# Optimization experiments

Measured on AMD Instinct MI355X. Metric: run time of the kernel, lower is better.

Reference implementation:

```python
import jax, jax.numpy as jnp
import numpy as np

B, D_IN, D_HID, D_OUT = 32768, 512, 4096, 512
EPS = 1e-12  # F.normalize eps


def setup_inputs() -> dict:
    key = jax.random.key(0)
    ks = jax.random.split(key, 9)
    # Weights scaled up from the original 0.001 init so the norm_max clamp
    # branch is actually exercised (norms vary around the threshold).
    return {
        "x": jax.random.normal(ks[0], (B, D_IN), jnp.float32),
        "in_mean": jax.random.normal(ks[1], (D_IN,), jnp.float32) * 0.1,
        "in_std": jax.random.uniform(ks[2], (D_IN,), jnp.float32, 0.5, 1.5),
        "out_mean": jax.random.normal(ks[3], (D_OUT,), jnp.float32) * 0.1,
        "out_std": jax.random.uniform(ks[4], (D_OUT,), jnp.float32, 0.5, 1.5),
        "W1": jax.random.normal(ks[5], (D_HID, D_IN), jnp.float32) * 0.02,
        "b1": jax.random.normal(ks[6], (D_HID,), jnp.float32) * 0.001,
        "W2": jax.random.normal(ks[7], (D_OUT, D_HID), jnp.float32) * 0.02,
        "b2": jax.random.normal(ks[8], (D_OUT,), jnp.float32) * 0.001,
        "norm_max": 1,
    }


def reference(x, in_mean, in_std, out_mean, out_std, W1, b1, W2, b2, norm_max):
    norm_max = jnp.float32(norm_max)
    x_copy = x[..., :512]
    # input normalization
    xn = (x - in_mean) / in_std
    # 2-layer MLP: Linear -> ReLU -> Linear
    h = jax.nn.relu(jnp.einsum("bi,hi->bh", xn, W1) + b1)
    res = jnp.einsum("bh,oh->bo", h, W2) + b2
    # vectorized per-row norm clamp (torch loop: rescale rows with norm > norm_max)
    norms = jnp.linalg.norm(res, axis=-1, keepdims=True)  # [B,1]
    scale = norm_max / jax.lax.stop_gradient(norms)
    res = jnp.where(norms > norm_max, res * scale, res)
    # output de-normalization (torch subtracts norm_input[0] here)
    res = res * out_std + out_mean - in_mean
    # residual + L2 normalize
    mapped = res + x_copy
    mnorm = jnp.linalg.norm(mapped, axis=-1, keepdims=True)
    return mapped / jnp.maximum(mnorm, EPS)
```

## Files before the change

### kernel.cpp

```cpp
#include <hip/hip_runtime.h>
#include <hip/hip_bf16.h>

#define NB 32768
#define DIN 512
#define DHID 4096
#define DOUT 512

typedef __attribute__((ext_vector_type(8))) __bf16 bf16x8;
typedef __attribute__((ext_vector_type(4))) float f32x4;

__device__ __forceinline__ unsigned short f2bf(float f) {
  unsigned u = __builtin_bit_cast(unsigned, f);
  u += 0x7FFFu + ((u >> 16) & 1u);
  return (unsigned short)(u >> 16);
}

__device__ __forceinline__ void gload16(void* lds, const void* g) {
  __builtin_amdgcn_global_load_lds(
      (const __attribute__((address_space(1))) void*)g,
      (__attribute__((address_space(3))) void*)lds, 16, 0, 0);
}

__global__ __launch_bounds__(256) void k_prep_x(
    const float4* __restrict__ x, const float* __restrict__ mean,
    const float* __restrict__ stdv, ushort4* __restrict__ xn) {
  const int i = blockIdx.x * 256 + threadIdx.x;
  const int col = (i << 2) & (DIN - 1);
  const float4 v = x[i];
  const float4 m = *(const float4*)(mean + col);
  const float4 s = *(const float4*)(stdv + col);
  ushort4 o;
  o.x = f2bf((v.x - m.x) / s.x);
  o.y = f2bf((v.y - m.y) / s.y);
  o.z = f2bf((v.z - m.z) / s.z);
  o.w = f2bf((v.w - m.w) / s.w);
  xn[i] = o;
}

__global__ __launch_bounds__(256) void k_cvt(
    const float4* __restrict__ in, ushort4* __restrict__ out) {
  const int i = blockIdx.x * 256 + threadIdx.x;
  const float4 v = in[i];
  ushort4 o;
  o.x = f2bf(v.x); o.y = f2bf(v.y); o.z = f2bf(v.z); o.w = f2bf(v.w);
  out[i] = o;
}

template <int EPI>
__global__ __launch_bounds__(512, 2) void k_gemm(
    const unsigned short* __restrict__ A, const unsigned short* __restrict__ W,
    const float* __restrict__ bias, void* __restrict__ outp,
    const int N, const int K, const int nbn) {
  __shared__ __align__(16) char lds[3 * 49152];
  const int tid = threadIdx.x;
  const int wave = tid >> 6, lane = tid & 63;
  const int wm = wave >> 1, wn = wave & 1;
  const int lidlo = lane & 15, lidhi = lane >> 4;

  const int nwg = (int)gridDim.x;
  const int wg = (int)blockIdx.x;
  const int q = nwg >> 3, r = nwg & 7;
  const int xcd = wg & 7, loc = wg >> 3;
  const int swz = (xcd < r ? xcd * (q + 1) : r * (q + 1) + (xcd - r) * q) + loc;
  const int bm = swz / nbn, bn = swz % nbn;
  const int R0 = bm * 256, C0 = bn * 128;

  const int NT = K >> 6;
  const int dbase0 = wave * 1024;

  auto STAGE = [&](int t, int s) {
    char* as = lds + s * 49152;
    char* bs = as + 32768;
    const int k0 = t << 6;
#pragma unroll
    for (int i = 0; i < 4; ++i) {
      const int db = i * 8192 + dbase0;
      const int d = db + lane * 16;
      const int row = d >> 7;
      const int colb = (d & 127) ^ ((row & 7) << 4);
      gload16(as + db,
              (const char*)A + ((size_t)(R0 + row) * K + k0) * 2 + colb);
    }
#pragma unroll
    for (int i = 0; i < 2; ++i) {
      const int db = i * 8192 + dbase0;
      const int d = db + lane * 16;
      const int row = d >> 7;
      const int colb = (d & 127) ^ ((row & 7) << 4);
      gload16(bs + db,
              (const char*)W + ((size_t)(C0 + row) * K + k0) * 2 + colb);
    }
  };

  f32x4 acc[4][4] = {};

  STAGE(0, 0);
  STAGE(1, 1);
  asm volatile("s_waitcnt vmcnt(6)" ::: "memory");
  __builtin_amdgcn_s_barrier();

  int slot = 0;
  for (int t = 0; t < NT; ++t) {
    const int nslot = (slot == 2) ? 0 : slot + 1;
    const int sslot = (nslot == 2) ? 0 : nslot + 1;
    if (t + 2 < NT) STAGE(t + 2, sslot);

    const char* as = lds + slot * 49152;
    const char* bs = as + 32768;
    bf16x8 af[2][4], bw[2][4];
#pragma unroll
    for (int kk = 0; kk < 2; ++kk) {
#pragma unroll
      for (int i = 0; i < 4; ++i) {
        const int ra = wm * 64 + i * 16 + lidlo;
        af[kk][i] = *(const bf16x8*)(
            as + ra * 128 + ((kk * 64 + lidhi * 16) ^ ((ra & 7) << 4)));
        const int rb = wn * 64 + i * 16 + lidlo;
        bw[kk][i] = *(const bf16x8*)(
            bs + rb * 128 + ((kk * 64 + lidhi * 16) ^ ((rb & 7) << 4)));
      }
    }
    __builtin_amdgcn_s_setprio(1);
#pragma unroll
    for (int kk = 0; kk < 2; ++kk)
#pragma unroll
      for (int i = 0; i < 4; ++i)
#pragma unroll
        for (int j = 0; j < 4; ++j)
          acc[i][j] = __builtin_amdgcn_mfma_f32_16x16x32_bf16(
              af[kk][i], bw[kk][j], acc[i][j], 0, 0, 0);
    __builtin_amdgcn_s_setprio(0);

    if (t + 2 < NT) {
      asm volatile("s_waitcnt vmcnt(6)" ::: "memory");
    } else {
      asm volatile("s_waitcnt vmcnt(0)" ::: "memory");
    }
    __builtin_amdgcn_s_barrier();
    slot = nslot;
  }

  const int m0 = R0 + wm * 64 + (lidhi << 2);
  const int n0 = C0 + wn * 64 + lidlo;
#pragma unroll
  for (int j = 0; j < 4; ++j) {
    const int n = n0 + j * 16;
    const float bv = bias[n];
#pragma unroll
    for (int i = 0; i < 4; ++i) {
#pragma unroll
      for (int rr = 0; rr < 4; ++rr) {
        const int m = m0 + i * 16 + rr;
        float v = acc[i][j][rr] + bv;
        if (EPI == 0) {
          v = fmaxf(v, 0.0f);
          ((unsigned short*)outp)[(size_t)m * N + n] = f2bf(v);
        } else {
          ((float*)outp)[(size_t)m * N + n] = v;
        }
      }
    }
  }
}

__global__ __launch_bounds__(256) void k_finalize(
    float* __restrict__ res, const float* __restrict__ x,
    const float* __restrict__ out_mean, const float* __restrict__ out_std,
    const float* __restrict__ in_mean, const int* __restrict__ nmp) {
  const int wave = threadIdx.x >> 6, lane = threadIdx.x & 63;
  const size_t row = (size_t)blockIdx.x * 4 + wave;
  const float nm = (float)(*nmp);
  const size_t base = row * DOUT + (size_t)lane * 8;
  const int c = lane * 8;
  const float4 r0 = *(const float4*)(res + base);
  const float4 r1 = *(const float4*)(res + base + 4);
  float ss = r0.x * r0.x + r0.y * r0.y + r0.z * r0.z + r0.w * r0.w +
             r1.x * r1.x + r1.y * r1.y + r1.z * r1.z + r1.w * r1.w;
#pragma unroll
  for (int o = 32; o > 0; o >>= 1) ss += __shfl_xor(ss, o);
  const float rn = sqrtf(ss);
  const float sc = (rn > nm) ? (nm / rn) : 1.0f;
  const float4 os0 = *(const float4*)(out_std + c);
  const float4 os1 = *(const float4*)(out_std + c + 4);
  const float4 om0 = *(const float4*)(out_mean + c);
  const float4 om1 = *(const float4*)(out_mean + c + 4);
  const float4 im0 = *(const float4*)(in_mean + c);
  const float4 im1 = *(const float4*)(in_mean + c + 4);
  const float4 x0 = *(const float4*)(x + base);
  const float4 x1 = *(const float4*)(x + base + 4);
  float4 m0, m1;
  m0.x = r0.x * sc * os0.x + om0.x - im0.x + x0.x;
  m0.y = r0.y * sc * os0.y + om0.y - im0.y + x0.y;
  m0.z = r0.z * sc * os0.z + om0.z - im0.z + x0.z;
  m0.w = r0.w * sc * os0.w + om0.w - im0.w + x0.w;
  m1.x = r1.x * sc * os1.x + om1.x - im1.x + x1.x;
  m1.y = r1.y * sc * os1.y + om1.y - im1.y + x1.y;
  m1.z = r1.z * sc * os1.z + om1.z - im1.z + x1.z;
  m1.w = r1.w * sc * os1.w + om1.w - im1.w + x1.w;
  float s2 = m0.x * m0.x + m0.y * m0.y + m0.z * m0.z + m0.w * m0.w +
             m1.x * m1.x + m1.y * m1.y + m1.z * m1.z + m1.w * m1.w;
#pragma unroll
  for (int o = 32; o > 0; o >>= 1) s2 += __shfl_xor(s2, o);
  const float inv = 1.0f / fmaxf(sqrtf(s2), 1e-12f);
  float4 o0, o1;
  o0.x = m0.x * inv; o0.y = m0.y * inv; o0.z = m0.z * inv; o0.w = m0.w * inv;
  o1.x = m1.x * inv; o1.y = m1.y * inv; o1.z = m1.z * inv; o1.w = m1.w * inv;
  *(float4*)(res + base) = o0;
  *(float4*)(res + base + 4) = o1;
}

extern "C" void kernel_launch(void* const* d_in, const int* in_sizes, int n_in,
                              void* d_out, int out_size, void* d_ws, size_t ws_size,
                              hipStream_t stream) {
  const float* x = (const float*)d_in[0];
  const float* in_mean = (const float*)d_in[1];
  const float* in_std = (const float*)d_in[2];
  const float* out_mean = (const float*)d_in[3];
  const float* out_std = (const float*)d_in[4];
  const float* W1 = (const float*)d_in[5];
  const float* b1 = (const float*)d_in[6];
  const float* W2 = (const float*)d_in[7];
  const float* b2 = (const float*)d_in[8];
  const int* nmp = (const int*)d_in[9];
  float* out = (float*)d_out;

  char* ws = (char*)d_ws;
  unsigned short* xn = (unsigned short*)ws;   ws += (size_t)NB * DIN * 2;
  unsigned short* W1b = (unsigned short*)ws;  ws += (size_t)DHID * DIN * 2;
  unsigned short* W2b = (unsigned short*)ws;  ws += (size_t)DOUT * DHID * 2;
  unsigned short* h = (unsigned short*)ws;

  const size_t fixedB = (size_t)(ws - (char*)d_ws);
  const size_t avail = (ws_size > fixedB) ? (ws_size - fixedB) : 0;
  long long crows = (long long)(avail / ((size_t)DHID * 2));
  if (crows > NB) crows = NB;
  crows &= ~255LL;
  if (crows < 256) crows = 256;
  const int chunk = (int)crows;

  k_prep_x<<<16384, 256, 0, stream>>>((const float4*)x, in_mean, in_std,
                                      (ushort4*)xn);
  k_cvt<<<2048, 256, 0, stream>>>((const float4*)W1, (ushort4*)W1b);
  k_cvt<<<2048, 256, 0, stream>>>((const float4*)W2, (ushort4*)W2b);

  for (int s = 0; s < NB; s += chunk) {
    const int mc = (NB - s < chunk) ? (NB - s) : chunk;
    const int g1 = (mc / 256) * (DHID / 128);
    k_gemm<0><<<g1, 512, 0, stream>>>(xn + (size_t)s * DIN, W1b, b1, (void*)h,
                                      DHID, DIN, DHID / 128);
    const int g2 = (mc / 256) * (DOUT / 128);
    k_gemm<1><<<g2, 512, 0, stream>>>(h, W2b, b2, (void*)(out + (size_t)s * DOUT),
                                      DOUT, DHID, DOUT / 128);
  }

  k_finalize<<<NB / 4, 256, 0, stream>>>(out, x, out_mean, out_std, in_mean, nmp);
}
```

Before: 468.0 us.

## Switch GEMM to 256x256 tiles with 32x32x16 MFMA and double buffering

The GEMM tile grows from 256x128 to 256x256 and the waves are rearranged into a 2x4 grid. Each wave now uses 32x32x16 bf16 MFMAs with 16-float accumulators instead of 16x16x32. The LDS layout changes to a k-chunk-major form without XOR swizzle, and the pipeline drops from three stages to two with a full vmcnt(0) wait every iteration. Occupancy goes from 2 workgroups per CU to 1. The larger tile increases operand reuse and cuts the LDS reads per MFMA, at the cost of occupancy, load-latency hiding, and fewer workgroups for the second GEMM (N=512 gives only 2 column tiles).

```diff
diff --git a/kernel.cpp b/kernel.cpp
--- a/kernel.cpp
+++ b/kernel.cpp
@@ -8,6 +8,7 @@
 
 typedef __attribute__((ext_vector_type(8))) __bf16 bf16x8;
 typedef __attribute__((ext_vector_type(4))) float f32x4;
+typedef __attribute__((ext_vector_type(16))) float f32x16;
 
 __device__ __forceinline__ unsigned short f2bf(float f) {
   unsigned u = __builtin_bit_cast(unsigned, f);
@@ -47,15 +48,15 @@
 }
 
 template <int EPI>
-__global__ __launch_bounds__(512, 2) void k_gemm(
+__global__ __launch_bounds__(512, 1) void k_gemm(
     const unsigned short* __restrict__ A, const unsigned short* __restrict__ W,
     const float* __restrict__ bias, void* __restrict__ outp,
     const int N, const int K, const int nbn) {
-  __shared__ __align__(16) char lds[3 * 49152];
+  __shared__ __align__(16) char lds[2 * 65536];
   const int tid = threadIdx.x;
   const int wave = tid >> 6, lane = tid & 63;
-  const int wm = wave >> 1, wn = wave & 1;
-  const int lidlo = lane & 15, lidhi = lane >> 4;
+  const int wm = wave >> 2, wn = wave & 3;
+  const int l31 = lane & 31, lhi = lane >> 5;
 
   const int nwg = (int)gridDim.x;
   const int wg = (int)blockIdx.x;
@@ -63,95 +64,81 @@
   const int xcd = wg & 7, loc = wg >> 3;
   const int swz = (xcd < r ? xcd * (q + 1) : r * (q + 1) + (xcd - r) * q) + loc;
   const int bm = swz / nbn, bn = swz % nbn;
-  const int R0 = bm * 256, C0 = bn * 128;
+  const int R0 = bm * 256, C0 = bn * 256;
 
   const int NT = K >> 6;
-  const int dbase0 = wave * 1024;
 
   auto STAGE = [&](int t, int s) {
-    char* as = lds + s * 49152;
+    char* as = lds + s * 65536;
     char* bs = as + 32768;
     const int k0 = t << 6;
 #pragma unroll
     for (int i = 0; i < 4; ++i) {
-      const int db = i * 8192 + dbase0;
-      const int d = db + lane * 16;
-      const int row = d >> 7;
-      const int colb = (d & 127) ^ ((row & 7) << 4);
-      gload16(as + db,
-              (const char*)A + ((size_t)(R0 + row) * K + k0) * 2 + colb);
-    }
-#pragma unroll
-    for (int i = 0; i < 2; ++i) {
-      const int db = i * 8192 + dbase0;
-      const int d = db + lane * 16;
-      const int row = d >> 7;
-      const int colb = (d & 127) ^ ((row & 7) << 4);
-      gload16(bs + db,
-              (const char*)W + ((size_t)(C0 + row) * K + k0) * 2 + colb);
+      const int c = wave * 4 + i;
+      const int kc = c >> 2;
+      const int row = ((c & 3) << 6) + lane;
+      gload16(as + c * 1024,
+              (const void*)(A + (size_t)(R0 + row) * K + k0 + kc * 8));
+    }
+#pragma unroll
+    for (int i = 0; i < 4; ++i) {
+      const int c = wave * 4 + i;
+      const int kc = c >> 2;
+      const int row = ((c & 3) << 6) + lane;
+      gload16(bs + c * 1024,
+              (const void*)(W + (size_t)(C0 + row) * K + k0 + kc * 8));
     }
   };
 
-  f32x4 acc[4][4] = {};
+  f32x16 acc[4][2] = {};
 
   STAGE(0, 0);
-  STAGE(1, 1);
-  asm volatile("s_waitcnt vmcnt(6)" ::: "memory");
+  asm volatile("s_waitcnt vmcnt(0)" ::: "memory");
   __builtin_amdgcn_s_barrier();
 
-  int slot = 0;
   for (int t = 0; t < NT; ++t) {
-    const int nslot = (slot == 2) ? 0 : slot + 1;
-    const int sslot = (nslot == 2) ? 0 : nslot + 1;
-    if (t + 2 < NT) STAGE(t + 2, sslot);
-
-    const char* as = lds + slot * 49152;
+    const int s = t & 1;
+    if (t + 1 < NT) STAGE(t + 1, s ^ 1);
+    const char* as = lds + s * 65536;
     const char* bs = as + 32768;
-    bf16x8 af[2][4], bw[2][4];
-#pragma unroll
-    for (int kk = 0; kk < 2; ++kk) {
-#pragma unroll
-      for (int i = 0; i < 4; ++i) {
-        const int ra = wm * 64 + i * 16 + lidlo;
-        af[kk][i] = *(const bf16x8*)(
-            as + ra * 128 + ((kk * 64 + lidhi * 16) ^ ((ra & 7) << 4)));
-        const int rb = wn * 64 + i * 16 + lidlo;
-        bw[kk][i] = *(const bf16x8*)(
-            bs + rb * 128 + ((kk * 64 + lidhi * 16) ^ ((rb & 7) << 4)));
-      }
-    }
-    __builtin_amdgcn_s_setprio(1);
-#pragma unroll
-    for (int kk = 0; kk < 2; ++kk)
-#pragma unroll
-      for (int i = 0; i < 4; ++i)
-#pragma unroll
-        for (int j = 0; j < 4; ++j)
-          acc[i][j] = __builtin_amdgcn_mfma_f32_16x16x32_bf16(
-              af[kk][i], bw[kk][j], acc[i][j], 0, 0, 0);
-    __builtin_amdgcn_s_setprio(0);
-
-    if (t + 2 < NT) {
-      asm volatile("s_waitcnt vmcnt(6)" ::: "memory");
-    } else {
-      asm volatile("s_waitcnt vmcnt(0)" ::: "memory");
-    }
+#pragma unroll
+    for (int ks = 0; ks < 4; ++ks) {
+      const int kc = ks * 2 + lhi;
+      bf16x8 af[4], bw[2];
+#pragma unroll
+      for (int mi = 0; mi < 4; ++mi)
+        af[mi] = *(const bf16x8*)(as + kc * 4096 +
+                                  (wm * 128 + mi * 32 + l31) * 16);
+#pragma unroll
+      for (int nj = 0; nj < 2; ++nj)
+        bw[nj] = *(const bf16x8*)(bs + kc * 4096 +
+                                  (wn * 64 + nj * 32 + l31) * 16);
+      __builtin_amdgcn_s_setprio(1);
+#pragma unroll
+      for (int mi = 0; mi < 4; ++mi)
+#pragma unroll
+        for (int nj = 0; nj < 2; ++nj)
+          acc[mi][nj] = __builtin_amdgcn_mfma_f32_32x32x16_bf16(
+              af[mi], bw[nj], acc[mi][nj], 0, 0, 0);
+      __builtin_amdgcn_s_setprio(0);
+    }
+    asm volatile("s_waitcnt vmcnt(0)" ::: "memory");
     __builtin_amdgcn_s_barrier();
-    slot = nslot;
   }
 
-  const int m0 = R0 + wm * 64 + (lidhi << 2);
-  const int n0 = C0 + wn * 64 + lidlo;
-#pragma unroll
-  for (int j = 0; j < 4; ++j) {
-    const int n = n0 + j * 16;
+  const int m_base = R0 + wm * 128;
+  const int n_base = C0 + wn * 64 + l31;
+#pragma unroll
+  for (int nj = 0; nj < 2; ++nj) {
+    const int n = n_base + nj * 32;
     const float bv = bias[n];
 #pragma unroll
-    for (int i = 0; i < 4; ++i) {
-#pragma unroll
-      for (int rr = 0; rr < 4; ++rr) {
-        const int m = m0 + i * 16 + rr;
-        float v = acc[i][j][rr] + bv;
+    for (int mi = 0; mi < 4; ++mi) {
+#pragma unroll
+      for (int reg = 0; reg < 16; ++reg) {
+        const int row = (reg & 3) + 8 * (reg >> 2) + 4 * lhi;
+        const int m = m_base + mi * 32 + row;
+        float v = acc[mi][nj][reg] + bv;
         if (EPI == 0) {
           v = fmaxf(v, 0.0f);
           ((unsigned short*)outp)[(size_t)m * N + n] = f2bf(v);
@@ -245,12 +232,12 @@
 
   for (int s = 0; s < NB; s += chunk) {
     const int mc = (NB - s < chunk) ? (NB - s) : chunk;
-    const int g1 = (mc / 256) * (DHID / 128);
+    const int g1 = (mc / 256) * (DHID / 256);
     k_gemm<0><<<g1, 512, 0, stream>>>(xn + (size_t)s * DIN, W1b, b1, (void*)h,
-                                      DHID, DIN, DHID / 128);
-    const int g2 = (mc / 256) * (DOUT / 128);
+                                      DHID, DIN, DHID / 256);
+    const int g2 = (mc / 256) * (DOUT / 256);
     k_gemm<1><<<g2, 512, 0, stream>>>(h, W2b, b2, (void*)(out + (size_t)s * DOUT),
-                                      DOUT, DHID, DOUT / 128);
+                                      DOUT, DHID, DOUT / 256);
   }
 
   k_finalize<<<NB / 4, 256, 0, stream>>>(out, x, out_mean, out_std, in_mean, nmp);
```

Measured after the change: 623.4 us. 33.2% more time.

## Add dedicated second GEMM with 128x512 full-width tiles and double buffering

Applied to the files above, without the earlier changes.

Replaces the templated second GEMM (256x128 tiles, grid over M and N) with a specialized kernel where each workgroup computes a 128-row by full 512-column output tile. The hidden activation A tile is then loaded once per row block instead of four times, which cuts global traffic for the large K=4096 operand. It uses two LDS stages of 80KB and 4x8 MFMA accumulators per wave. The costs are fewer workgroups (256 for the full batch), higher register pressure, and possibly lower occupancy given the large LDS use.

```diff
diff --git a/kernel.cpp b/kernel.cpp
--- a/kernel.cpp
+++ b/kernel.cpp
@@ -46,10 +46,9 @@
   out[i] = o;
 }
 
-template <int EPI>
-__global__ __launch_bounds__(512, 2) void k_gemm(
+__global__ __launch_bounds__(512, 2) void k_gemm1(
     const unsigned short* __restrict__ A, const unsigned short* __restrict__ W,
-    const float* __restrict__ bias, void* __restrict__ outp,
+    const float* __restrict__ bias, unsigned short* __restrict__ outp,
     const int N, const int K, const int nbn) {
   __shared__ __align__(16) char lds[3 * 49152];
   const int tid = threadIdx.x;
@@ -151,13 +150,104 @@
 #pragma unroll
       for (int rr = 0; rr < 4; ++rr) {
         const int m = m0 + i * 16 + rr;
-        float v = acc[i][j][rr] + bv;
-        if (EPI == 0) {
-          v = fmaxf(v, 0.0f);
-          ((unsigned short*)outp)[(size_t)m * N + n] = f2bf(v);
-        } else {
-          ((float*)outp)[(size_t)m * N + n] = v;
-        }
+        float v = fmaxf(acc[i][j][rr] + bv, 0.0f);
+        outp[(size_t)m * N + n] = f2bf(v);
+      }
+    }
+  }
+}
+
+__global__ __launch_bounds__(512, 2) void k_gemm2(
+    const unsigned short* __restrict__ A, const unsigned short* __restrict__ W,
+    const float* __restrict__ bias, float* __restrict__ outp, const int K) {
+  __shared__ __align__(16) char lds[2 * 81920];
+  const int tid = threadIdx.x;
+  const int wave = tid >> 6, lane = tid & 63;
+  const int wm = wave >> 2, wn = wave & 3;
+  const int lidlo = lane & 15, lidhi = lane >> 4;
+
+  const int nwg = (int)gridDim.x;
+  const int wg = (int)blockIdx.x;
+  const int q = nwg >> 3, r = nwg & 7;
+  const int xcd = wg & 7, loc = wg >> 3;
+  const int bm = (xcd < r ? xcd * (q + 1) : r * (q + 1) + (xcd - r) * q) + loc;
+  const int R0 = bm * 128;
+
+  const int NT = K >> 6;
+
+  auto STAGE = [&](int t, int s) {
+    char* as = lds + s * 81920;
+    char* bs = as + 16384;
+    const int k0 = t << 6;
+#pragma unroll
+    for (int i = 0; i < 10; ++i) {
+      const int c = wave * 10 + i;
+      if (c < 16) {
+        const int d = c * 1024 + lane * 16;
+        const int row = d >> 7;
+        const int colb = (d & 127) ^ ((row & 7) << 4);
+        gload16(as + c * 1024,
+                (const char*)A + ((size_t)(R0 + row) * K + k0) * 2 + colb);
+      } else {
+        const int d = (c - 16) * 1024 + lane * 16;
+        const int row = d >> 7;
+        const int colb = (d & 127) ^ ((row & 7) << 4);
+        gload16(bs + (c - 16) * 1024,
+                (const char*)W + ((size_t)row * K + k0) * 2 + colb);
+      }
+    }
+  };
+
+  f32x4 acc[4][8] = {};
+
+  STAGE(0, 0);
+  asm volatile("s_waitcnt vmcnt(0)" ::: "memory");
+  __builtin_amdgcn_s_barrier();
+
+  for (int t = 0; t < NT; ++t) {
+    if (t + 1 < NT) STAGE(t + 1, (t + 1) & 1);
+    const char* as = lds + (t & 1) * 81920;
+    const char* bs = as + 16384;
+#pragma unroll
+    for (int kk = 0; kk < 2; ++kk) {
+      bf16x8 af[4], bw[8];
+#pragma unroll
+      for (int i = 0; i < 4; ++i) {
+        const int ra = wm * 64 + i * 16 + lidlo;
+        af[i] = *(const bf16x8*)(
+            as + ra * 128 + ((kk * 64 + lidhi * 16) ^ ((ra & 7) << 4)));
+      }
+#pragma unroll
+      for (int j = 0; j < 8; ++j) {
+        const int rb = wn * 128 + j * 16 + lidlo;
+        bw[j] = *(const bf16x8*)(
+            bs + rb * 128 + ((kk * 64 + lidhi * 16) ^ ((rb & 7) << 4)));
+      }
+      __builtin_amdgcn_s_setprio(1);
+#pragma unroll
+      for (int i = 0; i < 4; ++i)
+#pragma unroll
+        for (int j = 0; j < 8; ++j)
+          acc[i][j] = __builtin_amdgcn_mfma_f32_16x16x32_bf16(
+              af[i], bw[j], acc[i][j], 0, 0, 0);
+      __builtin_amdgcn_s_setprio(0);
+    }
+    asm volatile("s_waitcnt vmcnt(0)" ::: "memory");
+    __builtin_amdgcn_s_barrier();
+  }
+
+  const int m0 = R0 + wm * 64 + (lidhi << 2);
+  const int n0 = wn * 128 + lidlo;
+#pragma unroll
+  for (int j = 0; j < 8; ++j) {
+    const int n = n0 + j * 16;
+    const float bv = bias[n];
+#pragma unroll
+    for (int i = 0; i < 4; ++i) {
+#pragma unroll
+      for (int rr = 0; rr < 4; ++rr) {
+        const int m = m0 + i * 16 + rr;
+        outp[(size_t)m * DOUT + n] = acc[i][j][rr] + bv;
       }
     }
   }
@@ -246,11 +336,10 @@
   for (int s = 0; s < NB; s += chunk) {
     const int mc = (NB - s < chunk) ? (NB - s) : chunk;
     const int g1 = (mc / 256) * (DHID / 128);
-    k_gemm<0><<<g1, 512, 0, stream>>>(xn + (size_t)s * DIN, W1b, b1, (void*)h,
-                                      DHID, DIN, DHID / 128);
-    const int g2 = (mc / 256) * (DOUT / 128);
-    k_gemm<1><<<g2, 512, 0, stream>>>(h, W2b, b2, (void*)(out + (size_t)s * DOUT),
-                                      DOUT, DHID, DOUT / 128);
+    k_gemm1<<<g1, 512, 0, stream>>>(xn + (size_t)s * DIN, W1b, b1, h,
+                                    DHID, DIN, DHID / 128);
+    const int g2 = mc / 128;
+    k_gemm2<<<g2, 512, 0, stream>>>(h, W2b, b2, out + (size_t)s * DOUT, DHID);
   }
 
   k_finalize<<<NB / 4, 256, 0, stream>>>(out, x, out_mean, out_std, in_mean, nmp);
```

After: 509.0 us. 1.09x slower.
